# Performance work log

Hardware: AMD Instinct MI355X
Metric: run time of the kernel (lower is better)

Reference implementation:

```python
import jax, jax.numpy as jnp
from jax import lax
import numpy as np

D_MODEL = 1024
D_STATE = 16
D_CONV = 4
EXPAND = 2
D_INNER = EXPAND * D_MODEL  # 2048
DT_RANK = D_MODEL // 16     # 64
BATCH = 4
SEQ = 1024


def setup_inputs() -> dict:
    key = jax.random.key(0)
    ks = iter(jax.random.split(key, 40))
    def w(shape, s=0.02):
        return (s * jax.random.normal(next(ks), shape)).astype(jnp.float32)
    inp = {"x": jax.random.normal(next(ks), (BATCH, SEQ, D_MODEL), dtype=jnp.float32)}
    # S4D-real style A init: A = -exp(A_log), A_log = log(1..N) per channel
    Alog = jnp.log(jnp.tile(jnp.arange(1, D_STATE + 1, dtype=jnp.float32), (D_INNER, 1)))
    for s in ("f", "b"):
        inp[f"inproj_{s}"] = w((D_MODEL, 2 * D_INNER))
        inp[f"conv_w_{s}"] = w((D_INNER, D_CONV), 0.2)
        inp[f"conv_b_{s}"] = jnp.zeros((D_INNER,), jnp.float32)
        inp[f"xproj_{s}"] = w((D_INNER, DT_RANK + 2 * D_STATE))
        inp[f"dt_w_{s}"] = w((DT_RANK, D_INNER))
        inp[f"dt_b_{s}"] = jnp.full((D_INNER,), -4.0, jnp.float32)  # softplus(-4)~0.018
        inp[f"Alog_{s}"] = Alog
        inp[f"Dp_{s}"] = jnp.ones((D_INNER,), jnp.float32)
        inp[f"outproj_{s}"] = w((D_INNER, D_MODEL))
    inp["gate_w"] = w((2 * D_MODEL, D_MODEL))
    inp["gate_b"] = jnp.zeros((D_MODEL,), jnp.float32)
    inp["proj_w"] = w((D_MODEL, D_MODEL))
    inp["proj_b"] = jnp.zeros((D_MODEL,), jnp.float32)
    return inp


def _mamba(x, inproj, conv_w, conv_b, xproj, dt_w, dt_b, Alog, Dp, outproj):
    B, L, _ = x.shape
    xz = x @ inproj                           # [B,L,2*Di]
    u, z = jnp.split(xz, 2, axis=-1)          # each [B,L,Di]
    # depthwise causal conv1d, width D_CONV
    K = conv_w.shape[1]
    up = jnp.pad(u, ((0, 0), (K - 1, 0), (0, 0)))
    uc = conv_b
    for k in range(K):
        uc = uc + up[:, k:k + L, :] * conv_w[:, k]
    uc = jax.nn.silu(uc)                      # [B,L,Di]
    dbl = uc @ xproj                          # [B,L,dt_rank+2N]
    N = Alog.shape[1]
    dt, Bm, Cm = jnp.split(dbl, [DT_RANK, DT_RANK + N], axis=-1)
    delta = jax.nn.softplus(dt @ dt_w + dt_b) # [B,L,Di]
    A = -jnp.exp(Alog)                        # [Di,N]

    def step(h, inp):
        u_t, d_t, B_t, C_t = inp              # [B,Di],[B,Di],[B,N],[B,N]
        dA = jnp.exp(d_t[..., None] * A)      # [B,Di,N]
        h = dA * h + (d_t * u_t)[..., None] * B_t[:, None, :]
        y_t = jnp.einsum('bdn,bn->bd', h, C_t)
        return h, y_t

    h0 = jnp.zeros((B, uc.shape[-1], N), x.dtype)
    xs = (uc.transpose(1, 0, 2), delta.transpose(1, 0, 2),
          Bm.transpose(1, 0, 2), Cm.transpose(1, 0, 2))
    _, ys = lax.scan(step, h0, xs)            # ys: [L,B,Di]
    y = ys.transpose(1, 0, 2) + uc * Dp
    y = y * jax.nn.silu(z)
    return y @ outproj                        # [B,L,d_model]


def reference(x, inproj_f, conv_w_f, conv_b_f, xproj_f, dt_w_f, dt_b_f, Alog_f, Dp_f, outproj_f,
              inproj_b, conv_w_b, conv_b_b, xproj_b, dt_w_b, dt_b_b, Alog_b, Dp_b, outproj_b,
              gate_w, gate_b, proj_w, proj_b):
    y_f = _mamba(x, inproj_f, conv_w_f, conv_b_f, xproj_f, dt_w_f, dt_b_f, Alog_f, Dp_f, outproj_f)
    xb = jnp.flip(x, axis=1)
    y_b = _mamba(xb, inproj_b, conv_w_b, conv_b_b, xproj_b, dt_w_b, dt_b_b, Alog_b, Dp_b, outproj_b)
    y_b = jnp.flip(y_b, axis=1)
    g = jax.nn.sigmoid(jnp.concatenate([y_f, y_b], axis=-1) @ gate_w + gate_b)
    y = g * y_f + (1.0 - g) * y_b
    return y @ proj_w + proj_b
```

## Files before the change

kernel.cpp:

```cpp
#include <hip/hip_runtime.h>
#include <hip/hip_bf16.h>

#define B_  4
#define L_  1024
#define DM  1024
#define DI  2048
#define NS  16
#define RK  64
#define MT  (B_ * L_)
#define NC  32
#define CH  (L_ / NC)
#define KSX 256
#define NZX 8
#define PSZ (B_ * NC * NS * DI)

typedef unsigned short u16;
typedef __attribute__((ext_vector_type(8))) short  bh8;
typedef __attribute__((ext_vector_type(8))) unsigned short us8;
typedef __attribute__((ext_vector_type(8))) _Float16 h8;
typedef __attribute__((ext_vector_type(4))) float  f4;

__device__ __forceinline__ float bf2f(u16 u) {
  union { unsigned int i; float f; } c; c.i = ((unsigned int)u) << 16; return c.f;
}
__device__ __forceinline__ u16 f2bf(float f) {
  union { float f; unsigned int i; } c; c.f = f;
  unsigned int x = c.i;
  unsigned int r = (x + 0x7fffu + ((x >> 16) & 1u)) >> 16;
  return (u16)r;
}

__device__ __forceinline__ void gl16(const u16* g, u16* l) {
  __builtin_amdgcn_global_load_lds(
      (const __attribute__((address_space(1))) void*)g,
      (__attribute__((address_space(3))) void*)l, 16, 0, 0);
}

__global__ void detect_k(const unsigned int* __restrict__ alog,
                         int* __restrict__ flag, int* __restrict__ afl) {
  *flag = (alog[0] != 0u) ? 1 : 0;
  afl[0] = 1; afl[1] = 1;
}

__global__ __launch_bounds__(256)
void cvt_k(const void* __restrict__ src, u16* __restrict__ dst, int n,
           const int* __restrict__ flag) {
  int i = blockIdx.x * 256 + threadIdx.x;
  if (i >= n) return;
  if (*flag) dst[i] = ((const u16*)src)[i];
  else       dst[i] = f2bf(((const float*)src)[i]);
}

__global__ __launch_bounds__(256)
void cvt10_k(const int* __restrict__ flagp,
             const void* s0, u16* d0, int n0, const void* s1, u16* d1, int n1,
             const void* s2, u16* d2, int n2, const void* s3, u16* d3, int n3,
             const void* s4, u16* d4, int n4, const void* s5, u16* d5, int n5,
             const void* s6, u16* d6, int n6, const void* s7, u16* d7, int n7,
             const void* s8, u16* d8, int n8, const void* s9, u16* d9, int n9)
{
  const void* s; u16* d; int n;
  switch (blockIdx.y) {
    case 0: s = s0; d = d0; n = n0; break;  case 1: s = s1; d = d1; n = n1; break;
    case 2: s = s2; d = d2; n = n2; break;  case 3: s = s3; d = d3; n = n3; break;
    case 4: s = s4; d = d4; n = n4; break;  case 5: s = s5; d = d5; n = n5; break;
    case 6: s = s6; d = d6; n = n6; break;  case 7: s = s7; d = d7; n = n7; break;
    case 8: s = s8; d = d8; n = n8; break;  default: s = s9; d = d9; n = n9; break;
  }
  int i = blockIdx.x * 256 + threadIdx.x;
  if (i >= n) return;
  d[i] = *flagp ? ((const u16*)s)[i] : f2bf(((const float*)s)[i]);
}

__global__ __launch_bounds__(256)
void a2_k(const int* __restrict__ flagp, const void* __restrict__ sf,
          const void* __restrict__ sb, _Float16* __restrict__ A2h,
          int* __restrict__ afl)
{
  int i = blockIdx.x * 256 + threadIdx.x;
  int dir = i >> 15;
  const void* src = dir ? sb : sf;
  int j = i & (DI * NS - 1);
  float v = *flagp ? bf2f(((const u16*)src)[j]) : ((const float*)src)[j];
  float a2 = -__expf(v);
  A2h[i] = (_Float16)a2;
  int n = i & 15;
  if (fabsf(a2 + (float)(n + 1)) > 1e-3f * (n + 1)) atomicAnd(&afl[dir], 0);
}

struct TpBatch {
  const void* src[8];
  u16* dst[8];
  int R[8], C[8], tilesX[8];
  int tOff[9];
  int cnt;
};

__global__ __launch_bounds__(256)
void tposeB_k(TpBatch tb, const int* __restrict__ flag) {
  __shared__ u16 tile[32][33];
  int bid = blockIdx.x;
  int i = 0;
  #pragma unroll
  for (int q = 0; q < 7; ++q) if (i + 1 < tb.cnt && bid >= tb.tOff[i + 1]) ++i;
  int local = bid - tb.tOff[i];
  int tX = tb.tilesX[i];
  int c0 = (local % tX) * 32, r0 = (local / tX) * 32;
  int R = tb.R[i], C = tb.C[i];
  const void* src = tb.src[i];
  u16* dst = tb.dst[i];
  int tx = threadIdx.x & 31, ty = threadIdx.x >> 5;
  int isbf = *flag;
  #pragma unroll
  for (int k = 0; k < 4; ++k) {
    int r = r0 + ty + k * 8, c = c0 + tx;
    u16 v = 0;
    if (r < R && c < C)
      v = isbf ? ((const u16*)src)[(size_t)r * C + c]
               : f2bf(((const float*)src)[(size_t)r * C + c]);
    tile[ty + k * 8][tx] = v;
  }
  __syncthreads();
  #pragma unroll
  for (int k = 0; k < 4; ++k) {
    int c = c0 + ty + k * 8, r = r0 + tx;
    if (c < C && r < R)
      dst[(size_t)c * R + r] = tile[tx][ty + k * 8];
  }
}

template<int ACT, int CATM, int OUTF, int BIDIR, int SPLITK, int DUO, int XSW, int ZDIR>
__global__ __launch_bounds__(256)
void gemm2(const u16* __restrict__ A, int lda,
           const u16* __restrict__ Wt,
           const u16* __restrict__ bias,
           void* __restrict__ Cp, int ldc, void* __restrict__ C2,
           int M, int N, int K,
           const u16* __restrict__ yfp, const u16* __restrict__ ybp,
           const int* __restrict__ flagp, const u16* __restrict__ Aalt)
{
  __shared__ __align__(16) u16 As[128][64];
  __shared__ __align__(16) u16 Bs[128][64];

  int bx, by;
  if (XSW) {
    int g = blockIdx.y * gridDim.x + blockIdx.x;
    int xcd = g & 7, j = g >> 3;
    int bxb = gridDim.x >> 3;
    int sh = 31 - __builtin_clz(bxb);
    bx = xcd * bxb + (j & (bxb - 1));
    by = j >> sh;
  } else { bx = blockIdx.x; by = blockIdx.y; }

  int zdir = 0, zslice = 0;
  if (ZDIR && SPLITK) { zdir = blockIdx.z >> 3; zslice = blockIdx.z & (NZX - 1); }
  else if (ZDIR)      { zdir = blockIdx.z; }
  else if (SPLITK)    { zslice = blockIdx.z; }

  const int tid  = threadIdx.x;
  const int lane = tid & 63;
  const int w    = tid >> 6;
  const int wm   = (w >> 1) * 64, wn = (w & 1) * 64;
  const int bm0  = by * 128, bn0 = bx * 128;
  const int l15  = lane & 15, quad = lane >> 4;
  const int rI8  = lane >> 3;
  const int cG8  = (lane & 7) ^ rI8;

  const u16* Wtp = ZDIR ? (Wt + (size_t)zdir * N * K) : Wt;

  f4 acc[4][4] = {};

  const int kb = SPLITK ? zslice * KSX : 0;
  const int ke = SPLITK ? kb + KSX : K;

  for (int k0 = kb; k0 < ke; k0 += 64) {
    {
      const u16* Abase;
      if (ZDIR)     Abase = zdir ? Aalt : A;
      else if (DUO) Abase = (bn0 < DM) ? A : ybp;
      else          Abase = A;
      #pragma unroll
      for (int t = 0; t < 4; ++t) {
        int rb = w * 32 + t * 8;
        int row = rb + rI8;
        const u16* gp;
        if (CATM) {
          int kk = k0 + cG8 * 8;
          int m = bm0 + row;
          gp = (kk < DM) ? (yfp + (size_t)m * DM + kk)
                         : (ybp + (size_t)(m ^ (L_ - 1)) * DM + (kk - DM));
        } else {
          gp = Abase + (size_t)(bm0 + row) * lda + k0 + cG8 * 8;
        }
        gl16(gp, &As[rb][0]);
      }
    }
    #pragma unroll
    for (int t = 0; t < 4; ++t) {
      int rb = w * 32 + t * 8;
      int row = rb + rI8;
      int n = bn0 + row; if (n > N - 1) n = N - 1;
      gl16(Wtp + (size_t)n * K + k0 + cG8 * 8, &Bs[rb][0]);
    }
    __syncthreads();
    #pragma unroll
    for (int s = 0; s < 2; ++s) {
      bh8 af[4], bg[4];
      const int phys = ((quad + 4 * s) ^ (l15 & 7)) * 8;
      #pragma unroll
      for (int i = 0; i < 4; ++i) {
        af[i] = *(const bh8*)&As[wm + i * 16 + l15][phys];
        bg[i] = *(const bh8*)&Bs[wn + i * 16 + l15][phys];
      }
      #pragma unroll
      for (int i = 0; i < 4; ++i)
        #pragma unroll
        for (int j = 0; j < 4; ++j)
          acc[i][j] = __builtin_amdgcn_mfma_f32_16x16x32_bf16(af[i], bg[j], acc[i][j], 0, 0, 0);
    }
    __syncthreads();
  }

  const int obf = (OUTF == 1) ? *flagp : 1;
  const size_t zoff = (OUTF == 2) ? (size_t)zslice * M * ldc : 0;
  #pragma unroll
  for (int j = 0; j < 4; ++j) {
    int lcol = bn0 + wn + j * 16 + l15;
    if (lcol >= N) continue;
    int col = BIDIR ? (lcol & 4095) : (DUO ? (lcol & (DM - 1)) : lcol);
    float bv = bias ? bf2f(bias[(ZDIR ? zdir * N : 0) + col]) : 0.f;
    #pragma unroll
    for (int i = 0; i < 4; ++i) {
      #pragma unroll
      for (int r = 0; r < 4; ++r) {
        int row = bm0 + wm + i * 16 + quad * 4 + r;
        float v = acc[i][j][r] + bv;
        if (ACT == 1) v = (v > 20.f) ? v : log1pf(__expf(v));
        if (ACT == 3) {
          float g = 1.f / (1.f + __expf(-v));
          float fv = bf2f(yfp[(size_t)row * DM + col]);
          float bb = bf2f(ybp[(size_t)(row ^ (L_ - 1)) * DM + col]);
          v = g * fv + (1.f - g) * bb;
        }
        if (OUTF == 2) {
          float* base = (ZDIR && zdir) ? (float*)C2 : (float*)Cp;
          base[zoff + (size_t)row * ldc + col] = v;
        } else if (BIDIR) {
          u16* base = (lcol < 4096) ? (u16*)Cp : (u16*)C2;
          int orow = (lcol < 4096) ? row : (row ^ (L_ - 1));
          u16* dst = (col < DI) ? (base + (size_t)orow * DI + col)
                                : (base + (size_t)(8u << 20) + (size_t)orow * DI + (col - DI));
          *dst = f2bf(v);
        } else if (DUO) {
          if (lcol < DM) ((u16*)Cp)[(size_t)row * ldc + col] = f2bf(v);
          else           ((u16*)C2)[(size_t)row * ldc + col] = f2bf(v);
        } else if (ZDIR) {
          u16* base = zdir ? (u16*)C2 : (u16*)Cp;
          base[(size_t)row * ldc + col] = f2bf(v);
        } else if (OUTF == 1 && !obf) {
          ((float*)Cp)[(size_t)row * ldc + col] = v;
        } else {
          ((u16*)Cp)[(size_t)row * ldc + col] = f2bf(v);
        }
      }
    }
  }
}

__global__ __launch_bounds__(512)
void gemm256i(const u16* __restrict__ A, int lda,
              const u16* __restrict__ Wt, int ldw,
              u16* __restrict__ Cp, u16* __restrict__ C2, int K)
{
  __shared__ __align__(16) u16 As[2][256][64];
  __shared__ __align__(16) u16 Bs[2][256][64];

  int g  = blockIdx.y * gridDim.x + blockIdx.x;
  int id = (g & 7) * ((gridDim.x * gridDim.y) >> 3) + (g >> 3);
  int bx = id >> 4;
  int by = id & 15;

  const int tid  = threadIdx.x;
  const int lane = tid & 63;
  const int w    = tid >> 6;
  const int wm2  = w >> 2;
  const int wn4  = w & 3;
  const int l15  = lane & 15, quad = lane >> 4;
  const int rI8  = lane >> 3;
  const int cG8  = (lane & 7) ^ rI8;
  const int bm0  = by * 256, bn0 = bx * 256;
  const int NT   = K >> 6;

  const u16* Ag = A  + (size_t)(bm0 + w * 8 + rI8) * lda + cG8 * 8;
  const u16* Bg = Wt + (size_t)(bn0 + w * 8 + rI8) * ldw + cG8 * 8;

  auto STAGE = [&](int kt, int bb) {
    const u16* ap = Ag + kt * 64;
    const u16* bp = Bg + kt * 64;
    #pragma unroll
    for (int i = 0; i < 4; ++i) {
      gl16(ap + (size_t)(i * 64) * lda, &As[bb][i * 64 + w * 8][0]);
      gl16(bp + (size_t)(i * 64) * ldw, &Bs[bb][i * 64 + w * 8][0]);
    }
  };

  f4 acc[8][4] = {};

  STAGE(0, 0);
  STAGE(1, 1);
  asm volatile("s_waitcnt vmcnt(8)" ::: "memory");
  __builtin_amdgcn_sched_barrier(0);
  __builtin_amdgcn_s_barrier();

  const int ph0 = ((quad    ) ^ (l15 & 7)) * 8;
  const int ph1 = ((quad + 4) ^ (l15 & 7)) * 8;

  for (int t = 0; t < NT; ++t) {
    const int bb = t & 1;
    bh8 af[4][2], bg[4][2], a2[4][2];

    #pragma unroll
    for (int x = 0; x < 4; ++x) {
      af[x][0] = *(const bh8*)&As[bb][wm2 * 128 + x * 16 + l15][ph0];
      af[x][1] = *(const bh8*)&As[bb][wm2 * 128 + x * 16 + l15][ph1];
    }
    #pragma unroll
    for (int x = 0; x < 2; ++x) {
      bg[x][0] = *(const bh8*)&Bs[bb][wn4 * 64 + x * 16 + l15][ph0];
      bg[x][1] = *(const bh8*)&Bs[bb][wn4 * 64 + x * 16 + l15][ph1];
    }
    __builtin_amdgcn_sched_barrier(0);
    __builtin_amdgcn_s_barrier();
    asm volatile("s_waitcnt lgkmcnt(0)" ::: "memory");
    __builtin_amdgcn_sched_barrier(0);
    __builtin_amdgcn_s_setprio(1);
    #pragma unroll
    for (int s = 0; s < 2; ++s)
      #pragma unroll
      for (int i = 0; i < 4; ++i)
        #pragma unroll
        for (int j = 0; j < 2; ++j)
          acc[i][j] = __builtin_amdgcn_mfma_f32_16x16x32_bf16(af[i][s], bg[j][s], acc[i][j], 0, 0, 0);
    __builtin_amdgcn_s_setprio(0);
    __builtin_amdgcn_sched_barrier(0);
    __builtin_amdgcn_s_barrier();

    #pragma unroll
    for (int x = 2; x < 4; ++x) {
      bg[x][0] = *(const bh8*)&Bs[bb][wn4 * 64 + x * 16 + l15][ph0];
      bg[x][1] = *(const bh8*)&Bs[bb][wn4 * 64 + x * 16 + l15][ph1];
    }
    __builtin_amdgcn_sched_barrier(0);
    __builtin_amdgcn_s_barrier();
    asm volatile("s_waitcnt lgkmcnt(0)" ::: "memory");
    __builtin_amdgcn_sched_barrier(0);
    __builtin_amdgcn_s_setprio(1);
    #pragma unroll
    for (int s = 0; s < 2; ++s)
      #pragma unroll
      for (int i = 0; i < 4; ++i)
        #pragma unroll
        for (int j = 0; j < 2; ++j)
          acc[i][2 + j] = __builtin_amdgcn_mfma_f32_16x16x32_bf16(af[i][s], bg[2 + j][s], acc[i][2 + j], 0, 0, 0);
    __builtin_amdgcn_s_setprio(0);
    __builtin_amdgcn_sched_barrier(0);
    __builtin_amdgcn_s_barrier();

    #pragma unroll
    for (int x = 0; x < 4; ++x) {
      a2[x][0] = *(const bh8*)&As[bb][wm2 * 128 + 64 + x * 16 + l15][ph0];
      a2[x][1] = *(const bh8*)&As[bb][wm2 * 128 + 64 + x * 16 + l15][ph1];
    }
    __builtin_amdgcn_sched_barrier(0);
    __builtin_amdgcn_s_barrier();
    asm volatile("s_waitcnt lgkmcnt(0)" ::: "memory");
    __builtin_amdgcn_sched_barrier(0);
    __builtin_amdgcn_s_setprio(1);
    #pragma unroll
    for (int s = 0; s < 2; ++s)
      #pragma unroll
      for (int i = 0; i < 4; ++i)
        #pragma unroll
        for (int j = 0; j < 2; ++j)
          acc[4 + i][j] = __builtin_amdgcn_mfma_f32_16x16x32_bf16(a2[i][s], bg[j][s], acc[4 + i][j], 0, 0, 0);
    __builtin_amdgcn_s_setprio(0);
    __builtin_amdgcn_sched_barrier(0);
    __builtin_amdgcn_s_barrier();

    if (t + 2 < NT) STAGE(t + 2, bb);
    __builtin_amdgcn_sched_barrier(0);
    __builtin_amdgcn_s_setprio(1);
    #pragma unroll
    for (int s = 0; s < 2; ++s)
      #pragma unroll
      for (int i = 0; i < 4; ++i)
        #pragma unroll
        for (int j = 0; j < 2; ++j)
          acc[4 + i][2 + j] = __builtin_amdgcn_mfma_f32_16x16x32_bf16(a2[i][s], bg[2 + j][s], acc[4 + i][2 + j], 0, 0, 0);
    __builtin_amdgcn_s_setprio(0);
    if (t + 2 < NT) { asm volatile("s_waitcnt vmcnt(8)" ::: "memory"); }
    else            { asm volatile("s_waitcnt vmcnt(0)" ::: "memory"); }
    __builtin_amdgcn_sched_barrier(0);
    __builtin_amdgcn_s_barrier();
  }

  {
    const int lc0  = bn0 + wn4 * 64;
    const int col0 = lc0 & 4095;
    u16* base = (lc0 < 4096) ? Cp : C2;
    u16* dst0 = (col0 < DI) ? base : (base + (size_t)(8u << 20) - DI);
    const int flip = (lc0 < 4096) ? 0 : (L_ - 1);
    #pragma unroll
    for (int i = 0; i < 8; ++i) {
      #pragma unroll
      for (int r = 0; r < 4; ++r) {
        int row = bm0 + wm2 * 128 + i * 16 + quad * 4 + r;
        u16* rp = dst0 + (size_t)(row ^ flip) * DI + col0;
        #pragma unroll
        for (int j = 0; j < 4; ++j)
          rp[j * 16 + l15] = f2bf(acc[i][j][r]);
      }
    }
  }
}

__global__ __launch_bounds__(256)
void rdbl_k(const float* __restrict__ xpf, const float* __restrict__ xpb,
            u16* __restrict__ dbl)
{
  int i = blockIdx.x * 256 + threadIdx.x;
  int dir = i >= MT * 96;
  int il = dir ? (i - MT * 96) : i;
  const float* P = dir ? xpb : xpf;
  float s = 0.f;
  #pragma unroll
  for (int z = 0; z < NZX; ++z) s += P[(size_t)z * MT * 96 + il];
  dbl[i] = f2bf(s);
}

__global__ __launch_bounds__(256)
void conv8_k(const u16* __restrict__ xzu_f, const u16* __restrict__ xzu_b,
             const u16* __restrict__ cw,
             const u16* __restrict__ cb,
             u16* __restrict__ uc)
{
  int g = blockIdx.x * 256 + threadIdx.x;
  int dir = g >> 20;
  int gl = g & ((1 << 20) - 1);
  int e = gl * 8;
  int d = e & (DI - 1);
  int t = (e >> 11) & (L_ - 1);
  int b = e >> 21;
  const u16* xzu = dir ? xzu_b : xzu_f;
  const u16* cwp = cw + dir * DI * 4;
  const u16* cbp = cb + dir * DI;
  float acc[8];
  us8 cbv = *(const us8*)&cbp[d];
  #pragma unroll
  for (int i = 0; i < 8; ++i) acc[i] = bf2f(cbv[i]);
  u16 wr[32];
  #pragma unroll
  for (int q = 0; q < 4; ++q)
    *(us8*)&wr[q * 8] = *(const us8*)&cwp[d * 4 + q * 8];
  #pragma unroll
  for (int k = 0; k < 4; ++k) {
    int ts = t + k - 3;
    if (ts >= 0) {
      us8 xv = *(const us8*)&xzu[(size_t)(b * L_ + ts) * DI + d];
      #pragma unroll
      for (int i = 0; i < 8; ++i)
        acc[i] += bf2f(xv[i]) * bf2f(wr[i * 4 + k]);
    }
  }
  us8 o;
  #pragma unroll
  for (int i = 0; i < 8; ++i)
    o[i] = f2bf(acc[i] / (1.f + __expf(-acc[i])));
  *(us8*)&uc[(size_t)dir * MT * DI + e] = o;
}

__global__ __launch_bounds__(256, 4)
void scanA_k(const u16* __restrict__ delta, const u16* __restrict__ uc,
             const u16* __restrict__ dbl, const _Float16* __restrict__ A2h,
             const int* __restrict__ afl,
             _Float16* __restrict__ P, _Float16* __restrict__ S)
{
  int g = blockIdx.x * 256 + threadIdx.x;
  int dir = g >> 18;
  int gl = g & ((1 << 18) - 1);
  int d = gl & (DI - 1);
  int c = (gl >> 11) & (NC - 1);
  int b = gl >> 16;
  delta += (size_t)dir * MT * DI;
  uc    += (size_t)dir * MT * DI;
  dbl   += (size_t)dir * MT * 96;
  P     += (size_t)dir * PSZ;
  S     += (size_t)dir * PSZ;
  const int fast = afl[dir];
  float A2[NS];
  if (!fast) {
    h8 a0 = *(const h8*)&A2h[((size_t)dir * DI + d) * NS];
    h8 a1 = *(const h8*)&A2h[((size_t)dir * DI + d) * NS + 8];
    #pragma unroll
    for (int n = 0; n < 8; ++n) { A2[n] = (float)a0[n]; A2[n + 8] = (float)a1[n]; }
  }
  float Pv[NS], Sv[NS];
  #pragma unroll
  for (int n = 0; n < NS; ++n) { Pv[n] = 1.f; Sv[n] = 0.f; }
  int t0 = c * CH;
  for (int t = t0; t < t0 + CH; ++t) {
    size_t row = (size_t)b * L_ + t;
    float dv = bf2f(delta[row * DI + d]);
    float uv = bf2f(uc[row * DI + d]);
    float du = dv * uv;
    us8 b0 = *(const us8*)&dbl[row * 96 + 64];
    us8 b1 = *(const us8*)&dbl[row * 96 + 72];
    if (fast) {
      float q = __expf(-dv);
      float dA = 1.f;
      #pragma unroll
      for (int n = 0; n < NS; ++n) {
        dA *= q;
        float Bv = (n < 8) ? bf2f(b0[n & 7]) : bf2f(b1[n & 7]);
        Sv[n] = fmaf(dA, Sv[n], du * Bv);
        Pv[n] *= dA;
      }
    } else {
      #pragma unroll
      for (int n = 0; n < NS; ++n) {
        float Bv = (n < 8) ? bf2f(b0[n & 7]) : bf2f(b1[n & 7]);
        float dA = __expf(dv * A2[n]);
        Sv[n] = fmaf(dA, Sv[n], du * Bv);
        Pv[n] *= dA;
      }
    }
  }
  size_t base = ((size_t)(b * NC + c) * NS) * DI + d;
  #pragma unroll
  for (int n = 0; n < NS; ++n) {
    P[base + (size_t)n * DI] = (_Float16)Pv[n];
    S[base + (size_t)n * DI] = (_Float16)Sv[n];
  }
}

__global__ __launch_bounds__(256)
void scanB_k(_Float16* __restrict__ P, const _Float16* __restrict__ S)
{
  int g = blockIdx.x * 256 + threadIdx.x;
  int dir = g >> 17;
  int gl = g & ((1 << 17) - 1);
  int d = gl & (DI - 1);
  int n = (gl >> 11) & (NS - 1);
  int b = gl >> 15;
  P += (size_t)dir * PSZ;
  S += (size_t)dir * PSZ;
  float h = 0.f;
  #pragma unroll 4
  for (int c = 0; c < NC; ++c) {
    size_t ix = ((size_t)(b * NC + c) * NS + n) * DI + d;
    float p = (float)P[ix], s = (float)S[ix];
    P[ix] = (_Float16)h;
    h = fmaf(p, h, s);
  }
}

__global__ __launch_bounds__(256, 4)
void scanC_k(const u16* __restrict__ uc, const u16* delta,
             const u16* __restrict__ dbl, const u16* __restrict__ xzz_f,
             const u16* __restrict__ xzz_b, const _Float16* __restrict__ A2h,
             const int* __restrict__ afl, const u16* __restrict__ Dp,
             const _Float16* __restrict__ hstart, u16* ys)
{
  int g = blockIdx.x * 256 + threadIdx.x;
  int dir = g >> 18;
  int gl = g & ((1 << 18) - 1);
  int d = gl & (DI - 1);
  int c = (gl >> 11) & (NC - 1);
  int b = gl >> 16;
  const u16* xzz = dir ? xzz_b : xzz_f;
  uc     += (size_t)dir * MT * DI;
  delta  += (size_t)dir * MT * DI;
  dbl    += (size_t)dir * MT * 96;
  Dp     += dir * DI;
  hstart += (size_t)dir * PSZ;
  ys     += (size_t)dir * MT * DI;
  const int fast = afl[dir];
  float A2[NS], h[NS];
  if (!fast) {
    h8 a0 = *(const h8*)&A2h[((size_t)dir * DI + d) * NS];
    h8 a1 = *(const h8*)&A2h[((size_t)dir * DI + d) * NS + 8];
    #pragma unroll
    for (int n = 0; n < 8; ++n) { A2[n] = (float)a0[n]; A2[n + 8] = (float)a1[n]; }
  }
  float Dv = bf2f(Dp[d]);
  size_t hbase = ((size_t)(b * NC + c) * NS) * DI + d;
  #pragma unroll
  for (int n = 0; n < NS; ++n) h[n] = (float)hstart[hbase + (size_t)n * DI];
  int t0 = c * CH;
  for (int t = t0; t < t0 + CH; ++t) {
    size_t row = (size_t)b * L_ + t;
    float dv = bf2f(delta[row * DI + d]);
    float uv = bf2f(uc[row * DI + d]);
    float du = dv * uv;
    us8 b0 = *(const us8*)&dbl[row * 96 + 64];
    us8 b1 = *(const us8*)&dbl[row * 96 + 72];
    us8 c0 = *(const us8*)&dbl[row * 96 + 80];
    us8 c1 = *(const us8*)&dbl[row * 96 + 88];
    float y = 0.f;
    if (fast) {
      float q = __expf(-dv);
      float dA = 1.f;
      #pragma unroll
      for (int n = 0; n < NS; ++n) {
        dA *= q;
        float Bv = (n < 8) ? bf2f(b0[n & 7]) : bf2f(b1[n & 7]);
        float Cv = (n < 8) ? bf2f(c0[n & 7]) : bf2f(c1[n & 7]);
        h[n] = fmaf(dA, h[n], du * Bv);
        y = fmaf(h[n], Cv, y);
      }
    } else {
      #pragma unroll
      for (int n = 0; n < NS; ++n) {
        float Bv = (n < 8) ? bf2f(b0[n & 7]) : bf2f(b1[n & 7]);
        float Cv = (n < 8) ? bf2f(c0[n & 7]) : bf2f(c1[n & 7]);
        float dA = __expf(dv * A2[n]);
        h[n] = fmaf(dA, h[n], du * Bv);
        y = fmaf(h[n], Cv, y);
      }
    }
    float z = bf2f(xzz[row * DI + d]);
    float out = (y + uv * Dv) * (z / (1.f + __expf(-z)));
    ys[row * DI + d] = f2bf(out);
  }
}

extern "C" void kernel_launch(void* const* d_in, const int* in_sizes, int n_in,
                              void* d_out, int out_size, void* d_ws, size_t ws_size,
                              hipStream_t stream)
{
  char* ws = (char*)d_ws;
  const size_t MB = 1ull << 20;
  const size_t KB = 1024;

  u16* xzu_f   = (u16*)(ws + 0);
  u16* xzz_f   = (u16*)(ws + 16 * MB);
  u16* xzu_b   = (u16*)(ws + 32 * MB);
  u16* xzz_b   = (u16*)(ws + 48 * MB);
  u16* uc      = (u16*)(ws + 64 * MB);
  u16* delta_f = (u16*)(ws + 96 * MB);
  u16* delta_b = (u16*)(ws + 112 * MB);
  u16* dbl     = (u16*)(ws + 128 * MB);
  char* SM     = ws + 128 * MB + 1536 * KB;
  u16* w_convw = (u16*)(SM);
  u16* w_convb = (u16*)(SM + 32 * KB);
  u16* w_dtb   = (u16*)(SM + 40 * KB);
  u16* w_dp    = (u16*)(SM + 48 * KB);
  u16* w_gb    = (u16*)(SM + 56 * KB);
  u16* w_pb    = (u16*)(SM + 58 * KB);
  int* flag    = (int*)(SM + 60 * KB);
  int* afl     = (int*)(SM + 60 * KB + 8);
  _Float16* A2h = (_Float16*)(ws + 128 * MB + 1600 * KB);
  u16* xproj_t2 = (u16*)(ws + 128 * MB + 1728 * KB);
  u16* dtw_t2   = (u16*)(ws + 128 * MB + 2496 * KB);
  u16* xc       = uc;
  u16* inproj_t = delta_f;
  float* xpart_f = (float*)delta_f;
  float* xpart_b = (float*)delta_b;
  _Float16* Pb   = (_Float16*)xzu_f;
  _Float16* Sb   = (_Float16*)xzu_b;
  u16* outp2_t  = (u16*)(ws + 80 * MB);
  u16* gw_t     = (u16*)(ws + 88 * MB);
  u16* pw_t     = (u16*)(ws + 92 * MB);
  u16* yf       = xzz_f;
  u16* yb       = xzz_b;
  u16* yc       = (u16*)(ws + 0);

  dim3 blk(256);
  detect_k<<<1, 1, 0, stream>>>((const unsigned int*)d_in[7], flag, afl);

  cvt10_k<<<dim3(32, 10), blk, 0, stream>>>(flag,
      d_in[2],  w_convw,            DI * 4, d_in[3],  w_convb,      DI,
      d_in[6],  w_dtb,              DI,     d_in[8],  w_dp,         DI,
      d_in[11], w_convw + DI * 4,   DI * 4, d_in[12], w_convb + DI, DI,
      d_in[15], w_dtb + DI,         DI,     d_in[17], w_dp + DI,    DI,
      d_in[20], w_gb,               DM,     d_in[22], w_pb,         DM);
  a2_k<<<2 * DI * NS / 256, blk, 0, stream>>>(flag, d_in[7], d_in[16], A2h, afl);
  cvt_k<<<MT * DM / 256, blk, 0, stream>>>(d_in[0], xc, MT * DM, flag);

  {
    TpBatch tb{};
    auto add = [&](int i, const void* s, u16* d, int R, int C) {
      tb.src[i] = s; tb.dst[i] = d; tb.R[i] = R; tb.C[i] = C;
      tb.tilesX[i] = (C + 31) / 32;
      tb.tOff[i + 1] = tb.tOff[i] + tb.tilesX[i] * ((R + 31) / 32);
    };
    tb.tOff[0] = 0;
    add(0, d_in[1],  inproj_t,               DM, 2 * DI);
    add(1, d_in[10], inproj_t + 4096 * 1024, DM, 2 * DI);
    add(2, d_in[4],  xproj_t2,               DI, 96);
    add(3, d_in[13], xproj_t2 + 96 * 2048,   DI, 96);
    add(4, d_in[5],  dtw_t2,                 RK, DI);
    add(5, d_in[14], dtw_t2 + 2048 * 64,     RK, DI);
    tb.cnt = 6;
    tposeB_k<<<tb.tOff[6], blk, 0, stream>>>(tb, flag);
  }

  gemm256i<<<dim3(32, 16), dim3(512), 0, stream>>>(
      xc, DM, inproj_t, DM, xzu_f, xzu_b, DM);

  conv8_k<<<2 * MT * DI / 8 / 256, blk, 0, stream>>>(
      xzu_f, xzu_b, w_convw, w_convb, uc);

  gemm2<0, 0, 2, 0, 1, 0, 0, 1><<<dim3(1, 32, 2 * NZX), blk, 0, stream>>>(
      uc, DI, xproj_t2, nullptr, xpart_f, 96, xpart_b, MT, 96, DI,
      nullptr, nullptr, flag, uc + (size_t)MT * DI);
  rdbl_k<<<2 * MT * 96 / 256, blk, 0, stream>>>(xpart_f, xpart_b, dbl);

  gemm2<1, 0, 0, 0, 0, 0, 1, 1><<<dim3(16, 32, 2), blk, 0, stream>>>(
      dbl, 96, dtw_t2, w_dtb, delta_f, DI, delta_b, MT, DI, RK,
      nullptr, nullptr, flag, dbl + (size_t)MT * 96);

  scanA_k<<<2 * B_ * NC * DI / 256, blk, 0, stream>>>(
      delta_f, uc, dbl, A2h, afl, Pb, Sb);
  scanB_k<<<2 * B_ * NS * DI / 256, blk, 0, stream>>>(Pb, Sb);
  scanC_k<<<2 * B_ * NC * DI / 256, blk, 0, stream>>>(
      uc, delta_f, dbl, xzz_f, xzz_b, A2h, afl, w_dp, Pb, delta_f);

  {
    TpBatch tb{};
    auto add = [&](int i, const void* s, u16* d, int R, int C) {
      tb.src[i] = s; tb.dst[i] = d; tb.R[i] = R; tb.C[i] = C;
      tb.tilesX[i] = (C + 31) / 32;
      tb.tOff[i + 1] = tb.tOff[i] + tb.tilesX[i] * ((R + 31) / 32);
    };
    tb.tOff[0] = 0;
    add(0, d_in[9],  outp2_t,               DI, DM);
    add(1, d_in[18], outp2_t + 1024 * 2048, DI, DM);
    add(2, d_in[19], gw_t,                  2 * DM, DM);
    add(3, d_in[21], pw_t,                  DM, DM);
    tb.cnt = 4;
    tposeB_k<<<tb.tOff[4], blk, 0, stream>>>(tb, flag);
  }

  gemm2<0, 0, 0, 0, 0, 1, 1, 0><<<dim3(16, 32), blk, 0, stream>>>(
      delta_f, DI, outp2_t, nullptr, yf, DM, yb, MT, 2 * DM, DI,
      nullptr, delta_b, flag, nullptr);

  gemm2<3, 1, 0, 0, 0, 0, 1, 0><<<dim3(8, 32), blk, 0, stream>>>(
      yf, DM, gw_t, w_gb, yc, DM, nullptr, MT, DM, 2 * DM, yf, yb, flag, nullptr);
  gemm2<0, 0, 1, 0, 0, 0, 1, 0><<<dim3(8, 32), blk, 0, stream>>>(
      yc, DM, pw_t, w_pb, d_out, DM, nullptr, MT, DM, DM,
      nullptr, nullptr, flag, nullptr);
}
```

Before: 618.8 us.

## Split GEMM tile prefetch into per-chunk loads interleaved across MFMA phases

The GEMM main loop used to prefetch whole K-tiles two steps ahead, issuing all A and B global-to-LDS loads in one burst before the last MFMA block. It now prefetches one step ahead and spreads individual 64-row chunks of B and A across the four MFMA phases. The vmcnt waits are retuned so each LDS region is complete just before it is read. This aims to smooth memory issue and overlap it better with compute, at the cost of a shallower prefetch that may leave global latency less hidden.

Result: no change. 611.6 us (-1.2%).

```diff
diff --git a/kernel.cpp b/kernel.cpp
--- a/kernel.cpp
+++ b/kernel.cpp
@@ -294,21 +294,18 @@
   const u16* Ag = A  + (size_t)(bm0 + w * 8 + rI8) * lda + cG8 * 8;
   const u16* Bg = Wt + (size_t)(bn0 + w * 8 + rI8) * ldw + cG8 * 8;
 
-  auto STAGE = [&](int kt, int bb) {
-    const u16* ap = Ag + kt * 64;
-    const u16* bp = Bg + kt * 64;
-    #pragma unroll
-    for (int i = 0; i < 4; ++i) {
-      gl16(ap + (size_t)(i * 64) * lda, &As[bb][i * 64 + w * 8][0]);
-      gl16(bp + (size_t)(i * 64) * ldw, &Bs[bb][i * 64 + w * 8][0]);
-    }
+  auto stA = [&](int kt, int bb, int c) {
+    gl16(Ag + kt * 64 + (size_t)(c * 64) * lda, &As[bb][c * 64 + w * 8][0]);
   };
+  auto stB = [&](int kt, int bb, int c) {
+    gl16(Bg + kt * 64 + (size_t)(c * 64) * ldw, &Bs[bb][c * 64 + w * 8][0]);
+  };
 
   f4 acc[8][4] = {};
 
-  STAGE(0, 0);
-  STAGE(1, 1);
-  asm volatile("s_waitcnt vmcnt(8)" ::: "memory");
+  stB(0, 0, 0); stB(0, 0, 1); stB(0, 0, 2); stB(0, 0, 3);
+  stA(0, 0, 0); stA(0, 0, 2); stA(0, 0, 1); stA(0, 0, 3);
+  asm volatile("s_waitcnt vmcnt(2)" ::: "memory");
   __builtin_amdgcn_sched_barrier(0);
   __builtin_amdgcn_s_barrier();
 
@@ -316,19 +313,22 @@
   const int ph1 = ((quad + 4) ^ (l15 & 7)) * 8;
 
   for (int t = 0; t < NT; ++t) {
-    const int bb = t & 1;
+    const int p = t & 1, q = p ^ 1;
+    const bool pre = (t + 1 < NT);
     bh8 af[4][2], bg[4][2], a2[4][2];
 
     #pragma unroll
     for (int x = 0; x < 4; ++x) {
-      af[x][0] = *(const bh8*)&As[bb][wm2 * 128 + x * 16 + l15][ph0];
-      af[x][1] = *(const bh8*)&As[bb][wm2 * 128 + x * 16 + l15][ph1];
+      af[x][0] = *(const bh8*)&As[p][wm2 * 128 + x * 16 + l15][ph0];
+      af[x][1] = *(const bh8*)&As[p][wm2 * 128 + x * 16 + l15][ph1];
     }
     #pragma unroll
     for (int x = 0; x < 2; ++x) {
-      bg[x][0] = *(const bh8*)&Bs[bb][wn4 * 64 + x * 16 + l15][ph0];
-      bg[x][1] = *(const bh8*)&Bs[bb][wn4 * 64 + x * 16 + l15][ph1];
-    }
+      bg[x][0] = *(const bh8*)&Bs[p][wn4 * 64 + x * 16 + l15][ph0];
+      bg[x][1] = *(const bh8*)&Bs[p][wn4 * 64 + x * 16 + l15][ph1];
+    }
+    if (pre) { stB(t + 1, q, 0); stB(t + 1, q, 1); }
+    asm volatile("s_waitcnt lgkmcnt(8)" ::: "memory");
     __builtin_amdgcn_sched_barrier(0);
     __builtin_amdgcn_s_barrier();
     asm volatile("s_waitcnt lgkmcnt(0)" ::: "memory");
@@ -347,9 +347,10 @@
 
     #pragma unroll
     for (int x = 2; x < 4; ++x) {
-      bg[x][0] = *(const bh8*)&Bs[bb][wn4 * 64 + x * 16 + l15][ph0];
-      bg[x][1] = *(const bh8*)&Bs[bb][wn4 * 64 + x * 16 + l15][ph1];
-    }
+      bg[x][0] = *(const bh8*)&Bs[p][wn4 * 64 + x * 16 + l15][ph0];
+      bg[x][1] = *(const bh8*)&Bs[p][wn4 * 64 + x * 16 + l15][ph1];
+    }
+    if (pre) { stB(t + 1, q, 2); stB(t + 1, q, 3); }
     __builtin_amdgcn_sched_barrier(0);
     __builtin_amdgcn_s_barrier();
     asm volatile("s_waitcnt lgkmcnt(0)" ::: "memory");
@@ -363,14 +364,17 @@
         for (int j = 0; j < 2; ++j)
           acc[i][2 + j] = __builtin_amdgcn_mfma_f32_16x16x32_bf16(af[i][s], bg[2 + j][s], acc[i][2 + j], 0, 0, 0);
     __builtin_amdgcn_s_setprio(0);
+    if (pre) { asm volatile("s_waitcnt vmcnt(4)" ::: "memory"); }
+    else     { asm volatile("s_waitcnt vmcnt(0)" ::: "memory"); }
     __builtin_amdgcn_sched_barrier(0);
     __builtin_amdgcn_s_barrier();
 
     #pragma unroll
     for (int x = 0; x < 4; ++x) {
-      a2[x][0] = *(const bh8*)&As[bb][wm2 * 128 + 64 + x * 16 + l15][ph0];
-      a2[x][1] = *(const bh8*)&As[bb][wm2 * 128 + 64 + x * 16 + l15][ph1];
-    }
+      a2[x][0] = *(const bh8*)&As[p][wm2 * 128 + 64 + x * 16 + l15][ph0];
+      a2[x][1] = *(const bh8*)&As[p][wm2 * 128 + 64 + x * 16 + l15][ph1];
+    }
+    if (pre) { stA(t + 1, q, 0); stA(t + 1, q, 2); }
     __builtin_amdgcn_sched_barrier(0);
     __builtin_amdgcn_s_barrier();
     asm volatile("s_waitcnt lgkmcnt(0)" ::: "memory");
@@ -387,7 +391,7 @@
     __builtin_amdgcn_sched_barrier(0);
     __builtin_amdgcn_s_barrier();
 
-    if (t + 2 < NT) STAGE(t + 2, bb);
+    if (pre) { stA(t + 1, q, 1); stA(t + 1, q, 3); }
     __builtin_amdgcn_sched_barrier(0);
     __builtin_amdgcn_s_setprio(1);
     #pragma unroll
@@ -398,8 +402,8 @@
         for (int j = 0; j < 2; ++j)
           acc[4 + i][2 + j] = __builtin_amdgcn_mfma_f32_16x16x32_bf16(a2[i][s], bg[2 + j][s], acc[4 + i][2 + j], 0, 0, 0);
     __builtin_amdgcn_s_setprio(0);
-    if (t + 2 < NT) { asm volatile("s_waitcnt vmcnt(8)" ::: "memory"); }
-    else            { asm volatile("s_waitcnt vmcnt(0)" ::: "memory"); }
+    if (pre) { asm volatile("s_waitcnt vmcnt(2)" ::: "memory"); }
+    else     { asm volatile("s_waitcnt vmcnt(0)" ::: "memory"); }
     __builtin_amdgcn_sched_barrier(0);
     __builtin_amdgcn_s_barrier();
   }
```

## Restructure GEMM main loop with register-prefetched fragments and single barrier per tile

Applied to the files above, without the earlier changes.

Rewrites the bf16 MFMA GEMM k-loop. It now prefetches only one tile ahead into the alternate LDS buffer, software-pipelines the LDS fragment reads into registers, and reorders the MFMA groups by k-half. The aim is to remove the four block barriers per iteration and hide LDS read latency behind the MFMAs. The cost is more live registers and a shorter global prefetch distance, with a full vmcnt(0) wait on every iteration.

Result: slower. 814.9 us (+31.7%).

```diff
diff --git a/kernel.cpp b/kernel.cpp
--- a/kernel.cpp
+++ b/kernel.cpp
@@ -306,102 +306,82 @@
 
   f4 acc[8][4] = {};
 
+  const int ph0 = ((quad    ) ^ (l15 & 7)) * 8;
+  const int ph1 = ((quad + 4) ^ (l15 & 7)) * 8;
+
   STAGE(0, 0);
-  STAGE(1, 1);
-  asm volatile("s_waitcnt vmcnt(8)" ::: "memory");
+  asm volatile("s_waitcnt vmcnt(0)" ::: "memory");
   __builtin_amdgcn_sched_barrier(0);
   __builtin_amdgcn_s_barrier();
-
-  const int ph0 = ((quad    ) ^ (l15 & 7)) * 8;
-  const int ph1 = ((quad + 4) ^ (l15 & 7)) * 8;
+  __builtin_amdgcn_sched_barrier(0);
+
+  bh8 aA[4], aB[4], aC[4], aD[4], bg0[4], bg1[4];
+  #pragma unroll
+  for (int x = 0; x < 4; ++x) {
+    aA[x]  = *(const bh8*)&As[0][wm2 * 128 + x * 16 + l15][ph0];
+    bg0[x] = *(const bh8*)&Bs[0][wn4 * 64  + x * 16 + l15][ph0];
+  }
 
   for (int t = 0; t < NT; ++t) {
-    const int bb = t & 1;
-    bh8 af[4][2], bg[4][2], a2[4][2];
+    const int p = t & 1, q = p ^ 1;
+    const bool pre = (t + 1 < NT);
+
+    if (pre) STAGE(t + 1, q);
+    #pragma unroll
+    for (int x = 0; x < 4; ++x)
+      aB[x] = *(const bh8*)&As[p][wm2 * 128 + 64 + x * 16 + l15][ph0];
+    __builtin_amdgcn_s_setprio(1);
+    #pragma unroll
+    for (int i = 0; i < 4; ++i)
+      #pragma unroll
+      for (int j = 0; j < 4; ++j)
+        acc[i][j] = __builtin_amdgcn_mfma_f32_16x16x32_bf16(aA[i], bg0[j], acc[i][j], 0, 0, 0);
+    __builtin_amdgcn_s_setprio(0);
 
     #pragma unroll
     for (int x = 0; x < 4; ++x) {
-      af[x][0] = *(const bh8*)&As[bb][wm2 * 128 + x * 16 + l15][ph0];
-      af[x][1] = *(const bh8*)&As[bb][wm2 * 128 + x * 16 + l15][ph1];
-    }
-    #pragma unroll
-    for (int x = 0; x < 2; ++x) {
-      bg[x][0] = *(const bh8*)&Bs[bb][wn4 * 64 + x * 16 + l15][ph0];
-      bg[x][1] = *(const bh8*)&Bs[bb][wn4 * 64 + x * 16 + l15][ph1];
-    }
-    __builtin_amdgcn_sched_barrier(0);
-    __builtin_amdgcn_s_barrier();
+      aC[x]  = *(const bh8*)&As[p][wm2 * 128 + x * 16 + l15][ph1];
+      bg1[x] = *(const bh8*)&Bs[p][wn4 * 64  + x * 16 + l15][ph1];
+    }
+    __builtin_amdgcn_s_setprio(1);
+    #pragma unroll
+    for (int i = 0; i < 4; ++i)
+      #pragma unroll
+      for (int j = 0; j < 4; ++j)
+        acc[4 + i][j] = __builtin_amdgcn_mfma_f32_16x16x32_bf16(aB[i], bg0[j], acc[4 + i][j], 0, 0, 0);
+    __builtin_amdgcn_s_setprio(0);
+
+    #pragma unroll
+    for (int x = 0; x < 4; ++x)
+      aD[x] = *(const bh8*)&As[p][wm2 * 128 + 64 + x * 16 + l15][ph1];
+    __builtin_amdgcn_s_setprio(1);
+    #pragma unroll
+    for (int i = 0; i < 4; ++i)
+      #pragma unroll
+      for (int j = 0; j < 4; ++j)
+        acc[i][j] = __builtin_amdgcn_mfma_f32_16x16x32_bf16(aC[i], bg1[j], acc[i][j], 0, 0, 0);
+    __builtin_amdgcn_s_setprio(0);
+
     asm volatile("s_waitcnt lgkmcnt(0)" ::: "memory");
     __builtin_amdgcn_sched_barrier(0);
+    if (pre) {
+      asm volatile("s_waitcnt vmcnt(0)" ::: "memory");
+      __builtin_amdgcn_sched_barrier(0);
+      __builtin_amdgcn_s_barrier();
+      __builtin_amdgcn_sched_barrier(0);
+      #pragma unroll
+      for (int x = 0; x < 4; ++x) {
+        aA[x]  = *(const bh8*)&As[q][wm2 * 128 + x * 16 + l15][ph0];
+        bg0[x] = *(const bh8*)&Bs[q][wn4 * 64  + x * 16 + l15][ph0];
+      }
+    }
     __builtin_amdgcn_s_setprio(1);
     #pragma unroll
-    for (int s = 0; s < 2; ++s)
-      #pragma unroll
-      for (int i = 0; i < 4; ++i)
-        #pragma unroll
-        for (int j = 0; j < 2; ++j)
-          acc[i][j] = __builtin_amdgcn_mfma_f32_16x16x32_bf16(af[i][s], bg[j][s], acc[i][j], 0, 0, 0);
+    for (int i = 0; i < 4; ++i)
+      #pragma unroll
+      for (int j = 0; j < 4; ++j)
+        acc[4 + i][j] = __builtin_amdgcn_mfma_f32_16x16x32_bf16(aD[i], bg1[j], acc[4 + i][j], 0, 0, 0);
     __builtin_amdgcn_s_setprio(0);
-    __builtin_amdgcn_sched_barrier(0);
-    __builtin_amdgcn_s_barrier();
-
-    #pragma unroll
-    for (int x = 2; x < 4; ++x) {
-      bg[x][0] = *(const bh8*)&Bs[bb][wn4 * 64 + x * 16 + l15][ph0];
-      bg[x][1] = *(const bh8*)&Bs[bb][wn4 * 64 + x * 16 + l15][ph1];
-    }
-    __builtin_amdgcn_sched_barrier(0);
-    __builtin_amdgcn_s_barrier();
-    asm volatile("s_waitcnt lgkmcnt(0)" ::: "memory");
-    __builtin_amdgcn_sched_barrier(0);
-    __builtin_amdgcn_s_setprio(1);
-    #pragma unroll
-    for (int s = 0; s < 2; ++s)
-      #pragma unroll
-      for (int i = 0; i < 4; ++i)
-        #pragma unroll
-        for (int j = 0; j < 2; ++j)
-          acc[i][2 + j] = __builtin_amdgcn_mfma_f32_16x16x32_bf16(af[i][s], bg[2 + j][s], acc[i][2 + j], 0, 0, 0);
-    __builtin_amdgcn_s_setprio(0);
-    __builtin_amdgcn_sched_barrier(0);
-    __builtin_amdgcn_s_barrier();
-
-    #pragma unroll
-    for (int x = 0; x < 4; ++x) {
-      a2[x][0] = *(const bh8*)&As[bb][wm2 * 128 + 64 + x * 16 + l15][ph0];
-      a2[x][1] = *(const bh8*)&As[bb][wm2 * 128 + 64 + x * 16 + l15][ph1];
-    }
-    __builtin_amdgcn_sched_barrier(0);
-    __builtin_amdgcn_s_barrier();
-    asm volatile("s_waitcnt lgkmcnt(0)" ::: "memory");
-    __builtin_amdgcn_sched_barrier(0);
-    __builtin_amdgcn_s_setprio(1);
-    #pragma unroll
-    for (int s = 0; s < 2; ++s)
-      #pragma unroll
-      for (int i = 0; i < 4; ++i)
-        #pragma unroll
-        for (int j = 0; j < 2; ++j)
-          acc[4 + i][j] = __builtin_amdgcn_mfma_f32_16x16x32_bf16(a2[i][s], bg[j][s], acc[4 + i][j], 0, 0, 0);
-    __builtin_amdgcn_s_setprio(0);
-    __builtin_amdgcn_sched_barrier(0);
-    __builtin_amdgcn_s_barrier();
-
-    if (t + 2 < NT) STAGE(t + 2, bb);
-    __builtin_amdgcn_sched_barrier(0);
-    __builtin_amdgcn_s_setprio(1);
-    #pragma unroll
-    for (int s = 0; s < 2; ++s)
-      #pragma unroll
-      for (int i = 0; i < 4; ++i)
-        #pragma unroll
-        for (int j = 0; j < 2; ++j)
-          acc[4 + i][2 + j] = __builtin_amdgcn_mfma_f32_16x16x32_bf16(a2[i][s], bg[2 + j][s], acc[4 + i][2 + j], 0, 0, 0);
-    __builtin_amdgcn_s_setprio(0);
-    if (t + 2 < NT) { asm volatile("s_waitcnt vmcnt(8)" ::: "memory"); }
-    else            { asm volatile("s_waitcnt vmcnt(0)" ::: "memory"); }
-    __builtin_amdgcn_sched_barrier(0);
-    __builtin_amdgcn_s_barrier();
   }
 
   {
```
